# Performance work log

Measured on AMD Instinct MI355X. Metric: run time of the kernel, lower is better.

The kernel has to match this reference:

```python
import jax, jax.numpy as jnp
import numpy as np

N = 262144
D = 1024
H = 512
B = 512  # number of bags / segments


def setup_inputs() -> dict:
    key = jax.random.key(0)
    k1, k2, k3, k4, k5 = jax.random.split(key, 5)
    x = jax.random.normal(k1, (N, D), dtype=jnp.float32)
    batch = jnp.sort(jax.random.randint(k2, (N,), 0, B, dtype=jnp.int64))
    s1 = 1.0 / np.sqrt(D)
    s3 = 1.0 / np.sqrt(H)
    W1 = jax.random.uniform(k3, (H, D), dtype=jnp.float32, minval=-s1, maxval=s1)
    W2 = jax.random.uniform(k4, (H, D), dtype=jnp.float32, minval=-s1, maxval=s1)
    W3 = jax.random.uniform(k5, (1, H), dtype=jnp.float32, minval=-s3, maxval=s3)
    return {"x": x, "batch": batch, "W1": W1, "W2": W2, "W3": W3}


def reference(x, batch, W1, W2, W3):
    # gated attention logits: tanh(x W1^T) * softmax_over_h(x W2^T) -> W3
    ux = jnp.tanh(x @ W1.T)                       # (n, h)
    vx = jax.nn.softmax(x @ W2.T, axis=1)         # (n, h), Softmax(dim=1)
    alpha = (ux * vx) @ W3.T                      # (n, 1)

    # segment-wise stable softmax over instances within each bag
    a = alpha[:, 0]                               # (n,)
    seg_max = jax.ops.segment_max(a, batch, num_segments=B)   # (B,)
    e = jnp.exp(a - seg_max[batch])               # (n,)
    seg_sum = jax.ops.segment_sum(e, batch, num_segments=B)   # (B,)
    w = e / seg_sum[batch]                        # (n,)

    # weighted segment add-pool: (B, d)
    z = jax.ops.segment_sum(x * w[:, None], batch, num_segments=B)
    return z
```

## Files before the change

### kernel.cpp

```cpp
#include <hip/hip_runtime.h>
#include <stdint.h>

#define N_ROWS 262144
#define D_DIM  1024
#define H_DIM  512
#define N_SEG  512

typedef __attribute__((ext_vector_type(4)))  float  f32x4;
typedef __attribute__((ext_vector_type(8)))  __bf16 bf16x8;
typedef __attribute__((ext_vector_type(8)))  unsigned short u16x8;

static __device__ __forceinline__ unsigned short c2bf(float f) {
  union { __bf16 b; unsigned short u; } c; c.b = (__bf16)f; return c.u;
}
static __device__ __forceinline__ float fast_tanh(float u) {
  return 1.0f - 2.0f / (__expf(2.0f * u) + 1.0f);
}

__global__ void cvt_w(const float* __restrict__ W1, const float* __restrict__ W2,
                      unsigned short* __restrict__ wbf) {
  int gid = blockIdx.x * 256 + threadIdx.x;
  int l   = gid & 63;
  int cfi = (gid >> 6) & 15;
  int kt  = (gid >> 10) & 31;
  int hs  = gid >> 15;
  int c   = (cfi << 4) + (l & 15);
  int h   = (hs << 7) + (c >> 1);
  int k0  = (kt << 5) + ((l >> 4) << 3);
  const float* src = ((c & 1) ? W2 : W1) + h * 1024 + k0;
  f32x4 f0 = *(const f32x4*)src;
  f32x4 f1 = *(const f32x4*)(src + 4);
  u16x8 v;
  v[0]=c2bf(f0[0]); v[1]=c2bf(f0[1]); v[2]=c2bf(f0[2]); v[3]=c2bf(f0[3]);
  v[4]=c2bf(f1[0]); v[5]=c2bf(f1[1]); v[6]=c2bf(f1[2]); v[7]=c2bf(f1[3]);
  *(u16x8*)(wbf + (size_t)gid * 8) = v;
}

#define MF(A, B, C) __builtin_amdgcn_mfma_f32_16x16x32_bf16((A), (B), (C), 0, 0, 0)

#define STAGEB(KT, BOFF) do { \
  __builtin_amdgcn_global_load_lds( \
    (const __attribute__((address_space(1))) void*)(wsrc + ((uint32_t)(KT) << 13)), \
    (__attribute__((address_space(3))) void*)(lds + (BOFF) + (wid << 11)), 16, 0, 0); \
  __builtin_amdgcn_global_load_lds( \
    (const __attribute__((address_space(1))) void*)(wsrc + ((uint32_t)(KT) << 13) + 512), \
    (__attribute__((address_space(3))) void*)(lds + (BOFF) + (wid << 11) + 1024), 16, 0, 0); \
} while (0)

#define ALOAD(KT) do { \
  rA0 = *(const f32x4*)(xsrc + ((KT) << 5)); \
  rA1 = *(const f32x4*)(xsrc + ((KT) << 5) + 4); \
} while (0)

#define PACKA(BOFF) do { \
  u16x8 va; \
  va[0]=c2bf(rA0[0]); va[1]=c2bf(rA0[1]); va[2]=c2bf(rA0[2]); va[3]=c2bf(rA0[3]); \
  va[4]=c2bf(rA1[0]); va[5]=c2bf(rA1[1]); va[6]=c2bf(rA1[2]); va[7]=c2bf(rA1[3]); \
  *(u16x8*)(lds + (BOFF) + (tid << 4)) = va; \
} while (0)

#define COMPUTE(ABUF, BBUF) do { \
  bf16x8 bf_[4], af[4]; \
  _Pragma("unroll") \
  for (int fc = 0; fc < 4; ++fc) \
    bf_[fc] = *(const bf16x8*)(lds + (BBUF) + (((cg << 2) + fc) << 10) + (lane << 4)); \
  _Pragma("unroll") \
  for (int fr = 0; fr < 4; ++fr) \
    af[fr] = *(const bf16x8*)(lds + (ABUF) + (((rg << 2) + fr) << 10) + (lane << 4)); \
  __builtin_amdgcn_s_setprio(1); \
  _Pragma("unroll") \
  for (int fr = 0; fr < 4; ++fr) \
    _Pragma("unroll") \
    for (int fc = 0; fc < 4; ++fc) \
      acc[fr][fc] = MF(af[fr], bf_[fc], acc[fr][fc]); \
  __builtin_amdgcn_s_setprio(0); \
} while (0)

#define BAR2() do { \
  asm volatile("s_waitcnt vmcnt(2) lgkmcnt(0)" ::: "memory"); \
  __builtin_amdgcn_s_barrier(); \
} while (0)
#define BAR0() do { \
  asm volatile("s_waitcnt vmcnt(0) lgkmcnt(0)" ::: "memory"); \
  __builtin_amdgcn_s_barrier(); \
} while (0)

__launch_bounds__(512, 4)
__global__ void alpha_kernel(const float* __restrict__ x,
                             const unsigned short* __restrict__ wbf,
                             const float* __restrict__ W3,
                             float* __restrict__ pm, float* __restrict__ ps,
                             float* __restrict__ pn)
{
  __shared__ unsigned char lds[49152];
  const int tid  = threadIdx.x;
  const int lane = tid & 63;
  const int wid  = tid >> 6;
  const int rg   = wid >> 2;
  const int cg   = wid & 3;
  const int l15  = lane & 15;
  const int lg   = lane >> 4;
  const int bid  = blockIdx.x;
  const int rt   = ((bid >> 5) << 3) + (bid & 7);
  const int hs   = (bid >> 3) & 3;
  const int row0 = rt << 7;

  const float* xsrc = x + (size_t)(row0 + ((tid >> 6) << 4) + (tid & 15)) * 1024
                        + (((tid >> 4) & 3) << 3);

  const unsigned short* wsrc = wbf + ((uint32_t)hs << 18) + ((uint32_t)wid << 10) + ((uint32_t)lane << 3);

  f32x4 acc[4][4];
  #pragma unroll
  for (int fr = 0; fr < 4; ++fr)
    #pragma unroll
    for (int fc = 0; fc < 4; ++fc) acc[fr][fc] = (f32x4){0.f, 0.f, 0.f, 0.f};

  f32x4 rA0, rA1;

  STAGEB(0, 16384);
  ALOAD(0);
  PACKA(0);
  ALOAD(1);
  BAR2();

  #pragma unroll 1
  for (int kt = 0; kt < 30; kt += 2) {
    STAGEB(kt + 1, 32768);
    COMPUTE(0, 16384);
    PACKA(8192);
    ALOAD(kt + 2);
    BAR2();
    STAGEB(kt + 2, 16384);
    COMPUTE(8192, 32768);
    PACKA(0);
    ALOAD(kt + 3);
    BAR2();
  }
  STAGEB(31, 32768);
  COMPUTE(0, 16384);
  PACKA(8192);
  BAR0();
  COMPUTE(8192, 32768);

  float w3v[4];
  #pragma unroll
  for (int fc = 0; fc < 4; ++fc)
    w3v[fc] = W3[(hs << 7) + (((cg << 6) + (fc << 4) + l15) >> 1)];

  float* pmb = (float*)(lds);
  float* psb = pmb + 512;
  float* pnb = psb + 512;

  #pragma unroll
  for (int fr = 0; fr < 4; ++fr) {
    f32x4 mv, sv, nv;
    #pragma unroll
    for (int j = 0; j < 4; ++j) {
      float g0 = fast_tanh(acc[fr][0][j]) * w3v[0];
      float g1 = fast_tanh(acc[fr][1][j]) * w3v[1];
      float g2 = fast_tanh(acc[fr][2][j]) * w3v[2];
      float g3 = fast_tanh(acc[fr][3][j]) * w3v[3];
      float gs0 = __shfl_xor(g0, 1);
      float gs1 = __shfl_xor(g1, 1);
      float gs2 = __shfl_xor(g2, 1);
      float gs3 = __shfl_xor(g3, 1);
      float mj = fmaxf(fmaxf(acc[fr][0][j], acc[fr][1][j]),
                       fmaxf(acc[fr][2][j], acc[fr][3][j]));
      mj = fmaxf(mj, __shfl_xor(mj, 2));
      mj = fmaxf(mj, __shfl_xor(mj, 4));
      mj = fmaxf(mj, __shfl_xor(mj, 8));
      float p0 = __expf(acc[fr][0][j] - mj);
      float p1 = __expf(acc[fr][1][j] - mj);
      float p2 = __expf(acc[fr][2][j] - mj);
      float p3 = __expf(acc[fr][3][j] - mj);
      float sj = p0 + p1 + p2 + p3;
      float nj = gs0 * p0 + gs1 * p1 + gs2 * p2 + gs3 * p3;
      sj += __shfl_xor(sj, 2); nj += __shfl_xor(nj, 2);
      sj += __shfl_xor(sj, 4); nj += __shfl_xor(nj, 4);
      sj += __shfl_xor(sj, 8); nj += __shfl_xor(nj, 8);
      mv[j] = mj; sv[j] = sj; nv[j] = nj;
    }
    if (l15 == 1) {
      int idx = (cg << 7) + (rg << 6) + (fr << 4) + (lg << 2);
      *(f32x4*)&pmb[idx] = mv;
      *(f32x4*)&psb[idx] = sv;
      *(f32x4*)&pnb[idx] = nv;
    }
  }
  __syncthreads();
  if (tid < 128) {
    float m0 = pmb[tid], m1 = pmb[128 + tid], m2 = pmb[256 + tid], m3 = pmb[384 + tid];
    float M = fmaxf(fmaxf(m0, m1), fmaxf(m2, m3));
    float e0 = __expf(m0 - M), e1 = __expf(m1 - M), e2 = __expf(m2 - M), e3 = __expf(m3 - M);
    float S  = psb[tid]*e0 + psb[128+tid]*e1 + psb[256+tid]*e2 + psb[384+tid]*e3;
    float Nn = pnb[tid]*e0 + pnb[128+tid]*e1 + pnb[256+tid]*e2 + pnb[384+tid]*e3;
    size_t r = (size_t)(row0 + tid);
    pm[r * 4 + hs] = M;
    ps[r * 4 + hs] = S;
    pn[r * 4 + hs] = Nn;
  }
}

__global__ void combine_a(const float* __restrict__ pm, const float* __restrict__ ps,
                          const float* __restrict__ pn, float* __restrict__ a) {
  size_t r = (size_t)blockIdx.x * 256 + threadIdx.x;
  float M = -3.4e38f;
  #pragma unroll
  for (int s = 0; s < 4; ++s) M = fmaxf(M, pm[r * 4 + s]);
  float S = 0.f, Nn = 0.f;
  #pragma unroll
  for (int s = 0; s < 4; ++s) {
    float e = __expf(pm[r * 4 + s] - M);
    S  += ps[r * 4 + s] * e;
    Nn += pn[r * 4 + s] * e;
  }
  a[r] = Nn / S;
}

static __device__ __forceinline__ int lower_bound(const int* __restrict__ batch, int key) {
  int lo = 0, hi = N_ROWS;
  while (lo < hi) { int mid = (lo + hi) >> 1; if (batch[mid] < key) lo = mid + 1; else hi = mid; }
  return lo;
}

__global__ void seg_kernel(const float* __restrict__ a, const int* __restrict__ batch,
                           float* __restrict__ w) {
  __shared__ float sm[8];
  int b = blockIdx.x;
  int start = lower_bound(batch, b);
  int end   = lower_bound(batch, b + 1);
  int tid = threadIdx.x;

  float m = -3.4e38f;
  for (int i = start + tid; i < end; i += 256) m = fmaxf(m, a[i]);
  for (int d = 1; d < 64; d <<= 1) m = fmaxf(m, __shfl_xor(m, d));
  if ((tid & 63) == 0) sm[tid >> 6] = m;
  __syncthreads();
  m = fmaxf(fmaxf(sm[0], sm[1]), fmaxf(sm[2], sm[3]));

  float s = 0.f;
  for (int i = start + tid; i < end; i += 256) s += __expf(a[i] - m);
  for (int d = 1; d < 64; d <<= 1) s += __shfl_xor(s, d);
  if ((tid & 63) == 0) sm[4 + (tid >> 6)] = s;
  __syncthreads();
  s = sm[4] + sm[5] + sm[6] + sm[7];

  float rinv = 1.0f / s;
  for (int i = start + tid; i < end; i += 256) w[i] = __expf(a[i] - m) * rinv;
}

__global__ void z_kernel(const float* __restrict__ x, const float* __restrict__ w,
                         const int* __restrict__ batch, float* __restrict__ z) {
  int b = blockIdx.x >> 2, part = blockIdx.x & 3;
  int start = lower_bound(batch, b);
  int end   = lower_bound(batch, b + 1);
  int len = end - start;
  int ps = start + ((len * part) >> 2);
  int pe = start + ((len * (part + 1)) >> 2);
  int col = threadIdx.x << 2;

  f32x4 acc = (f32x4){0.f, 0.f, 0.f, 0.f};
  for (int i = ps; i < pe; ++i) {
    f32x4 xv = *(const f32x4*)(x + ((size_t)i << 10) + col);
    float wi = w[i];
    acc += xv * wi;
  }
  float* zp = z + ((size_t)b << 10) + col;
  atomicAdd(zp + 0, acc[0]);
  atomicAdd(zp + 1, acc[1]);
  atomicAdd(zp + 2, acc[2]);
  atomicAdd(zp + 3, acc[3]);
}

extern "C" void kernel_launch(void* const* d_in, const int* in_sizes, int n_in,
                              void* d_out, int out_size, void* d_ws, size_t ws_size,
                              hipStream_t stream) {
  const float* x     = (const float*)d_in[0];
  const int*   batch = (const int*)d_in[1];
  const float* W1    = (const float*)d_in[2];
  const float* W2    = (const float*)d_in[3];
  const float* W3    = (const float*)d_in[4];
  float* z = (float*)d_out;

  unsigned short* wbf = (unsigned short*)d_ws;
  float* a  = (float*)((char*)d_ws + (2u << 20));
  float* w  = (float*)((char*)d_ws + (3u << 20));
  float* pm = (float*)((char*)d_ws + (4u << 20));
  float* ps = (float*)((char*)d_ws + (8u << 20));
  float* pn = (float*)((char*)d_ws + (12u << 20));

  (void)hipMemsetAsync(d_out, 0, (size_t)N_SEG * D_DIM * sizeof(float), stream);

  cvt_w<<<512, 256, 0, stream>>>(W1, W2, wbf);

  alpha_kernel<<<8192, 512, 0, stream>>>(x, wbf, W3, pm, ps, pn);

  combine_a<<<N_ROWS / 256, 256, 0, stream>>>(pm, ps, pn, a);

  seg_kernel<<<N_SEG, 256, 0, stream>>>(a, batch, w);

  z_kernel<<<N_SEG * 4, 256, 0, stream>>>(x, w, batch, z);
}
```

Before: 1.035 ms.

## Split each K-step into two barrier-ping-ponged MFMA half-phases interleaved with loads

Restructures the main GEMM loop so each K-tile is processed in two halves: load B fragments and half of A, issue the next B stage, run 8 MFMAs, then load the rest of A, pack and issue the next A global load, and run the remaining 8 MFMAs. Extra s_barriers are inserted around each half to create a ping-pong schedule where waves alternate between memory and MFMA work. The goal is better overlap of LDS and global traffic with matrix compute, at the cost of more barriers and finer-grained synchronization that could stall waves.

```diff
diff --git a/kernel.cpp b/kernel.cpp
--- a/kernel.cpp
+++ b/kernel.cpp
@@ -59,14 +59,43 @@
   *(u16x8*)(lds + (BOFF) + (tid << 4)) = va; \
 } while (0)
 
+#define LDB(BUF, FC) (*(const bf16x8*)(lds + (BUF) + (((cg << 2) + (FC)) << 10) + (lane << 4)))
+#define LDA(BUF, FR) (*(const bf16x8*)(lds + (BUF) + (((rg << 2) + (FR)) << 10) + (lane << 4)))
+
+#define PHASE(ABUF, BBUF, AOTH, BOTH, KT) do { \
+  bf16x8 bf0 = LDB(BBUF, 0), bf1 = LDB(BBUF, 1), bf2 = LDB(BBUF, 2), bf3 = LDB(BBUF, 3); \
+  bf16x8 a0 = LDA(ABUF, 0), a1 = LDA(ABUF, 1); \
+  STAGEB((KT) + 1, BOTH); \
+  __builtin_amdgcn_s_barrier(); \
+  asm volatile("s_waitcnt lgkmcnt(0)" ::: "memory"); \
+  __builtin_amdgcn_s_setprio(1); \
+  acc[0][0] = MF(a0, bf0, acc[0][0]); acc[0][1] = MF(a0, bf1, acc[0][1]); \
+  acc[0][2] = MF(a0, bf2, acc[0][2]); acc[0][3] = MF(a0, bf3, acc[0][3]); \
+  acc[1][0] = MF(a1, bf0, acc[1][0]); acc[1][1] = MF(a1, bf1, acc[1][1]); \
+  acc[1][2] = MF(a1, bf2, acc[1][2]); acc[1][3] = MF(a1, bf3, acc[1][3]); \
+  __builtin_amdgcn_s_setprio(0); \
+  __builtin_amdgcn_s_barrier(); \
+  bf16x8 a2 = LDA(ABUF, 2), a3 = LDA(ABUF, 3); \
+  PACKA(AOTH); \
+  ALOAD((KT) + 2); \
+  __builtin_amdgcn_s_barrier(); \
+  asm volatile("s_waitcnt lgkmcnt(0)" ::: "memory"); \
+  __builtin_amdgcn_s_setprio(1); \
+  acc[2][0] = MF(a2, bf0, acc[2][0]); acc[2][1] = MF(a2, bf1, acc[2][1]); \
+  acc[2][2] = MF(a2, bf2, acc[2][2]); acc[2][3] = MF(a2, bf3, acc[2][3]); \
+  acc[3][0] = MF(a3, bf0, acc[3][0]); acc[3][1] = MF(a3, bf1, acc[3][1]); \
+  acc[3][2] = MF(a3, bf2, acc[3][2]); acc[3][3] = MF(a3, bf3, acc[3][3]); \
+  __builtin_amdgcn_s_setprio(0); \
+  asm volatile("s_waitcnt vmcnt(2)" ::: "memory"); \
+  __builtin_amdgcn_s_barrier(); \
+} while (0)
+
 #define COMPUTE(ABUF, BBUF) do { \
   bf16x8 bf_[4], af[4]; \
   _Pragma("unroll") \
-  for (int fc = 0; fc < 4; ++fc) \
-    bf_[fc] = *(const bf16x8*)(lds + (BBUF) + (((cg << 2) + fc) << 10) + (lane << 4)); \
+  for (int fc = 0; fc < 4; ++fc) bf_[fc] = LDB(BBUF, fc); \
   _Pragma("unroll") \
-  for (int fr = 0; fr < 4; ++fr) \
-    af[fr] = *(const bf16x8*)(lds + (ABUF) + (((rg << 2) + fr) << 10) + (lane << 4)); \
+  for (int fr = 0; fr < 4; ++fr) af[fr] = LDA(ABUF, fr); \
   __builtin_amdgcn_s_setprio(1); \
   _Pragma("unroll") \
   for (int fr = 0; fr < 4; ++fr) \
@@ -76,10 +105,6 @@
   __builtin_amdgcn_s_setprio(0); \
 } while (0)
 
-#define BAR2() do { \
-  asm volatile("s_waitcnt vmcnt(2) lgkmcnt(0)" ::: "memory"); \
-  __builtin_amdgcn_s_barrier(); \
-} while (0)
 #define BAR0() do { \
   asm volatile("s_waitcnt vmcnt(0) lgkmcnt(0)" ::: "memory"); \
   __builtin_amdgcn_s_barrier(); \
@@ -122,20 +147,13 @@
   ALOAD(0);
   PACKA(0);
   ALOAD(1);
-  BAR2();
+  asm volatile("s_waitcnt vmcnt(2) lgkmcnt(0)" ::: "memory");
+  __builtin_amdgcn_s_barrier();
 
   #pragma unroll 1
   for (int kt = 0; kt < 30; kt += 2) {
-    STAGEB(kt + 1, 32768);
-    COMPUTE(0, 16384);
-    PACKA(8192);
-    ALOAD(kt + 2);
-    BAR2();
-    STAGEB(kt + 2, 16384);
-    COMPUTE(8192, 32768);
-    PACKA(0);
-    ALOAD(kt + 3);
-    BAR2();
+    PHASE(0,    16384, 8192, 32768, kt);
+    PHASE(8192, 32768, 0,    16384, kt + 1);
   }
   STAGEB(31, 32768);
   COMPUTE(0, 16384);
```

After: 1.057 ms. +2.2%, slower.

## Pre-convert x to swizzled bf16 chunks and use 256-row tiles with triple-buffered DMA

Applied to the files above, without the earlier changes.

Adds a cvt_x pass that converts x in 16 chunks to bf16 in a swizzled tile layout, so the GEMM kernel can stage A via direct global-to-LDS loads instead of register load plus convert plus LDS store. The new alpha_fast kernel uses 256-row tiles (8x4 MFMA fragments per wave), 96KB dynamic LDS with triple buffering, and occupancy 2, which roughly halves redundant B traffic per row. The cost is an extra read of x in fp32 and a write and re-read of the bf16 copy, plus 32 extra launches. It only runs when the workspace is at least 56MB; otherwise the old kernel is used.

```diff
diff --git a/kernel.cpp b/kernel.cpp
--- a/kernel.cpp
+++ b/kernel.cpp
@@ -36,6 +36,27 @@
   *(u16x8*)(wbf + (size_t)gid * 8) = v;
 }
 
+__global__ void cvt_x(const float* __restrict__ x, unsigned short* __restrict__ ximg,
+                      int chunk) {
+  int gid = blockIdx.x * 256 + threadIdx.x;
+  int s   = gid & 1023;
+  int kt  = (gid >> 10) & 31;
+  int rtl = gid >> 15;
+  int f   = s >> 6;
+  int j   = s & 63;
+  int r4  = j >> 2;
+  int c   = j & 3;
+  int row = (((chunk << 6) + rtl) << 8) + (f << 4) + r4;
+  int k0  = (kt << 5) + ((c ^ (r4 & 3)) << 3);
+  const float* src = x + (size_t)row * 1024 + k0;
+  f32x4 f0 = *(const f32x4*)src;
+  f32x4 f1 = *(const f32x4*)(src + 4);
+  u16x8 v;
+  v[0]=c2bf(f0[0]); v[1]=c2bf(f0[1]); v[2]=c2bf(f0[2]); v[3]=c2bf(f0[3]);
+  v[4]=c2bf(f1[0]); v[5]=c2bf(f1[1]); v[6]=c2bf(f1[2]); v[7]=c2bf(f1[3]);
+  *(u16x8*)(ximg + (size_t)gid * 8) = v;
+}
+
 #define MF(A, B, C) __builtin_amdgcn_mfma_f32_16x16x32_bf16((A), (B), (C), 0, 0, 0)
 
 #define STAGEB(KT, BOFF) do { \
@@ -47,26 +68,175 @@
     (__attribute__((address_space(3))) void*)(lds + (BOFF) + (wid << 11) + 1024), 16, 0, 0); \
 } while (0)
 
-#define ALOAD(KT) do { \
+#define LDB(BUF, FC) (*(const bf16x8*)(lds + (BUF) + (((cg << 2) + (FC)) << 10) + (lane << 4)))
+
+#define FAST_A0 0
+#define FAST_A1 16384
+#define FAST_A2 32768
+#define FAST_B0 49152
+#define FAST_B1 65536
+#define FAST_B2 81920
+
+#define STAGEA(KT, AOFF) do { \
+  __builtin_amdgcn_global_load_lds( \
+    (const __attribute__((address_space(1))) void*)(asrc + ((uint32_t)(KT) << 13)), \
+    (__attribute__((address_space(3))) void*)(lds + (AOFF) + (wid << 10)), 16, 0, 0); \
+  __builtin_amdgcn_global_load_lds( \
+    (const __attribute__((address_space(1))) void*)(asrc + ((uint32_t)(KT) << 13) + 4096), \
+    (__attribute__((address_space(3))) void*)(lds + (AOFF) + (wid << 10) + 8192), 16, 0, 0); \
+} while (0)
+
+#define LDA8(BUF, FR) (*(const bf16x8*)(lds + (BUF) + (((rg << 3) + (FR)) << 10) + abase))
+
+#define MFQ16(FB, A0_, A1_, A2_, A3_) do { \
+  acc[(FB)+0][0]=MF(A0_,b0,acc[(FB)+0][0]); acc[(FB)+0][1]=MF(A0_,b1,acc[(FB)+0][1]); \
+  acc[(FB)+0][2]=MF(A0_,b2,acc[(FB)+0][2]); acc[(FB)+0][3]=MF(A0_,b3,acc[(FB)+0][3]); \
+  acc[(FB)+1][0]=MF(A1_,b0,acc[(FB)+1][0]); acc[(FB)+1][1]=MF(A1_,b1,acc[(FB)+1][1]); \
+  acc[(FB)+1][2]=MF(A1_,b2,acc[(FB)+1][2]); acc[(FB)+1][3]=MF(A1_,b3,acc[(FB)+1][3]); \
+  acc[(FB)+2][0]=MF(A2_,b0,acc[(FB)+2][0]); acc[(FB)+2][1]=MF(A2_,b1,acc[(FB)+2][1]); \
+  acc[(FB)+2][2]=MF(A2_,b2,acc[(FB)+2][2]); acc[(FB)+2][3]=MF(A2_,b3,acc[(FB)+2][3]); \
+  acc[(FB)+3][0]=MF(A3_,b0,acc[(FB)+3][0]); acc[(FB)+3][1]=MF(A3_,b1,acc[(FB)+3][1]); \
+  acc[(FB)+3][2]=MF(A3_,b2,acc[(FB)+3][2]); acc[(FB)+3][3]=MF(A3_,b3,acc[(FB)+3][3]); \
+} while (0)
+
+#define KTILE(RA, RB, SA, SB, KT, DOSTAGE, VMSTR) do { \
+  bf16x8 b0 = LDB(RB,0), b1 = LDB(RB,1), b2 = LDB(RB,2), b3 = LDB(RB,3); \
+  bf16x8 a0 = LDA8(RA,0), a1 = LDA8(RA,1), a2 = LDA8(RA,2), a3 = LDA8(RA,3); \
+  if (DOSTAGE) { STAGEA((KT)+2, SA); STAGEB((KT)+2, SB); } \
+  __builtin_amdgcn_s_barrier(); \
+  asm volatile("s_waitcnt lgkmcnt(0)" ::: "memory"); \
+  __builtin_amdgcn_s_setprio(1); MFQ16(0, a0, a1, a2, a3); __builtin_amdgcn_s_setprio(0); \
+  __builtin_amdgcn_s_barrier(); \
+  bf16x8 a4 = LDA8(RA,4), a5 = LDA8(RA,5), a6 = LDA8(RA,6), a7 = LDA8(RA,7); \
+  __builtin_amdgcn_s_barrier(); \
+  asm volatile("s_waitcnt lgkmcnt(0)" ::: "memory"); \
+  __builtin_amdgcn_s_setprio(1); MFQ16(4, a4, a5, a6, a7); __builtin_amdgcn_s_setprio(0); \
+  asm volatile("s_waitcnt vmcnt(" VMSTR ")" ::: "memory"); \
+  __builtin_amdgcn_s_barrier(); \
+} while (0)
+
+__launch_bounds__(512, 2)
+__global__ void alpha_fast(const unsigned short* __restrict__ ximg,
+                           const unsigned short* __restrict__ wbf,
+                           const float* __restrict__ W3,
+                           float* __restrict__ pm, float* __restrict__ ps,
+                           float* __restrict__ pn, int chunk)
+{
+  extern __shared__ unsigned char lds[];
+  const int tid  = threadIdx.x;
+  const int lane = tid & 63;
+  const int wid  = tid >> 6;
+  const int rg   = wid >> 2;
+  const int cg   = wid & 3;
+  const int l15  = lane & 15;
+  const int lg   = lane >> 4;
+  const int bid  = blockIdx.x;
+  const int rtl  = ((bid >> 5) << 3) + (bid & 7);
+  const int hs   = (bid >> 3) & 3;
+  const int rt   = (chunk << 6) + rtl;
+  const int row0 = rt << 8;
+
+  const unsigned short* asrc = ximg + ((size_t)rtl << 18) + ((uint32_t)tid << 3);
+  const unsigned short* wsrc = wbf + ((uint32_t)hs << 18) + ((uint32_t)wid << 10) + ((uint32_t)lane << 3);
+
+  const uint32_t abase = ((uint32_t)l15 << 6) + (((uint32_t)(lg ^ (l15 & 3))) << 4);
+
+  f32x4 acc[8][4];
+  #pragma unroll
+  for (int fr = 0; fr < 8; ++fr)
+    #pragma unroll
+    for (int fc = 0; fc < 4; ++fc) acc[fr][fc] = (f32x4){0.f, 0.f, 0.f, 0.f};
+
+  STAGEA(0, FAST_A0); STAGEB(0, FAST_B0);
+  STAGEA(1, FAST_A1); STAGEB(1, FAST_B1);
+  asm volatile("s_waitcnt vmcnt(4)" ::: "memory");
+  __builtin_amdgcn_s_barrier();
+
+  #pragma unroll 1
+  for (int kt = 0; kt < 30; kt += 3) {
+    KTILE(FAST_A0, FAST_B0, FAST_A2, FAST_B2, kt,     1, "4");
+    KTILE(FAST_A1, FAST_B1, FAST_A0, FAST_B0, kt + 1, 1, "4");
+    KTILE(FAST_A2, FAST_B2, FAST_A1, FAST_B1, kt + 2, 1, "4");
+  }
+  KTILE(FAST_A0, FAST_B0, FAST_A2, FAST_B2, 30, 0, "0");
+  KTILE(FAST_A1, FAST_B1, FAST_A2, FAST_B2, 31, 0, "0");
+
+  float w3v[4];
+  #pragma unroll
+  for (int fc = 0; fc < 4; ++fc)
+    w3v[fc] = W3[(hs << 7) + (((cg << 6) + (fc << 4) + l15) >> 1)];
+
+  float* pmb = (float*)(lds);
+  float* psb = pmb + 1024;
+  float* pnb = psb + 1024;
+
+  #pragma unroll
+  for (int fr = 0; fr < 8; ++fr) {
+    f32x4 mv, sv, nv;
+    #pragma unroll
+    for (int j = 0; j < 4; ++j) {
+      float g0 = fast_tanh(acc[fr][0][j]) * w3v[0];
+      float g1 = fast_tanh(acc[fr][1][j]) * w3v[1];
+      float g2 = fast_tanh(acc[fr][2][j]) * w3v[2];
+      float g3 = fast_tanh(acc[fr][3][j]) * w3v[3];
+      float gs0 = __shfl_xor(g0, 1);
+      float gs1 = __shfl_xor(g1, 1);
+      float gs2 = __shfl_xor(g2, 1);
+      float gs3 = __shfl_xor(g3, 1);
+      float mj = fmaxf(fmaxf(acc[fr][0][j], acc[fr][1][j]),
+                       fmaxf(acc[fr][2][j], acc[fr][3][j]));
+      mj = fmaxf(mj, __shfl_xor(mj, 2));
+      mj = fmaxf(mj, __shfl_xor(mj, 4));
+      mj = fmaxf(mj, __shfl_xor(mj, 8));
+      float p0 = __expf(acc[fr][0][j] - mj);
+      float p1 = __expf(acc[fr][1][j] - mj);
+      float p2 = __expf(acc[fr][2][j] - mj);
+      float p3 = __expf(acc[fr][3][j] - mj);
+      float sj = p0 + p1 + p2 + p3;
+      float nj = gs0 * p0 + gs1 * p1 + gs2 * p2 + gs3 * p3;
+      sj += __shfl_xor(sj, 2); nj += __shfl_xor(nj, 2);
+      sj += __shfl_xor(sj, 4); nj += __shfl_xor(nj, 4);
+      sj += __shfl_xor(sj, 8); nj += __shfl_xor(nj, 8);
+      mv[j] = mj; sv[j] = sj; nv[j] = nj;
+    }
+    if (l15 == 1) {
+      int idx = (cg << 8) + (rg << 7) + (fr << 4) + (lg << 2);
+      *(f32x4*)&pmb[idx] = mv;
+      *(f32x4*)&psb[idx] = sv;
+      *(f32x4*)&pnb[idx] = nv;
+    }
+  }
+  __syncthreads();
+  if (tid < 256) {
+    float m0 = pmb[tid], m1 = pmb[256 + tid], m2 = pmb[512 + tid], m3 = pmb[768 + tid];
+    float M = fmaxf(fmaxf(m0, m1), fmaxf(m2, m3));
+    float e0 = __expf(m0 - M), e1 = __expf(m1 - M), e2 = __expf(m2 - M), e3 = __expf(m3 - M);
+    float S  = psb[tid]*e0 + psb[256+tid]*e1 + psb[512+tid]*e2 + psb[768+tid]*e3;
+    float Nn = pnb[tid]*e0 + pnb[256+tid]*e1 + pnb[512+tid]*e2 + pnb[768+tid]*e3;
+    size_t r = (size_t)(row0 + tid);
+    pm[r * 4 + hs] = M;
+    ps[r * 4 + hs] = S;
+    pn[r * 4 + hs] = Nn;
+  }
+}
+
+#define FB_ALOAD(KT) do { \
   rA0 = *(const f32x4*)(xsrc + ((KT) << 5)); \
   rA1 = *(const f32x4*)(xsrc + ((KT) << 5) + 4); \
 } while (0)
-
-#define PACKA(BOFF) do { \
+#define FB_PACKA(BOFF) do { \
   u16x8 va; \
   va[0]=c2bf(rA0[0]); va[1]=c2bf(rA0[1]); va[2]=c2bf(rA0[2]); va[3]=c2bf(rA0[3]); \
   va[4]=c2bf(rA1[0]); va[5]=c2bf(rA1[1]); va[6]=c2bf(rA1[2]); va[7]=c2bf(rA1[3]); \
   *(u16x8*)(lds + (BOFF) + (tid << 4)) = va; \
 } while (0)
-
-#define COMPUTE(ABUF, BBUF) do { \
+#define FB_LDA(BUF, FR) (*(const bf16x8*)(lds + (BUF) + (((rg << 2) + (FR)) << 10) + (lane << 4)))
+#define FB_COMPUTE(ABUF, BBUF) do { \
   bf16x8 bf_[4], af[4]; \
   _Pragma("unroll") \
-  for (int fc = 0; fc < 4; ++fc) \
-    bf_[fc] = *(const bf16x8*)(lds + (BBUF) + (((cg << 2) + fc) << 10) + (lane << 4)); \
+  for (int fc = 0; fc < 4; ++fc) bf_[fc] = LDB(BBUF, fc); \
   _Pragma("unroll") \
-  for (int fr = 0; fr < 4; ++fr) \
-    af[fr] = *(const bf16x8*)(lds + (ABUF) + (((rg << 2) + fr) << 10) + (lane << 4)); \
+  for (int fr = 0; fr < 4; ++fr) af[fr] = FB_LDA(ABUF, fr); \
   __builtin_amdgcn_s_setprio(1); \
   _Pragma("unroll") \
   for (int fr = 0; fr < 4; ++fr) \
@@ -75,22 +245,21 @@
       acc[fr][fc] = MF(af[fr], bf_[fc], acc[fr][fc]); \
   __builtin_amdgcn_s_setprio(0); \
 } while (0)
-
-#define BAR2() do { \
+#define FB_BAR2() do { \
   asm volatile("s_waitcnt vmcnt(2) lgkmcnt(0)" ::: "memory"); \
   __builtin_amdgcn_s_barrier(); \
 } while (0)
-#define BAR0() do { \
+#define FB_BAR0() do { \
   asm volatile("s_waitcnt vmcnt(0) lgkmcnt(0)" ::: "memory"); \
   __builtin_amdgcn_s_barrier(); \
 } while (0)
 
 __launch_bounds__(512, 4)
-__global__ void alpha_kernel(const float* __restrict__ x,
-                             const unsigned short* __restrict__ wbf,
-                             const float* __restrict__ W3,
-                             float* __restrict__ pm, float* __restrict__ ps,
-                             float* __restrict__ pn)
+__global__ void alpha_fb(const float* __restrict__ x,
+                         const unsigned short* __restrict__ wbf,
+                         const float* __restrict__ W3,
+                         float* __restrict__ pm, float* __restrict__ ps,
+                         float* __restrict__ pn)
 {
   __shared__ unsigned char lds[49152];
   const int tid  = threadIdx.x;
@@ -107,7 +276,6 @@
 
   const float* xsrc = x + (size_t)(row0 + ((tid >> 6) << 4) + (tid & 15)) * 1024
                         + (((tid >> 4) & 3) << 3);
-
   const unsigned short* wsrc = wbf + ((uint32_t)hs << 18) + ((uint32_t)wid << 10) + ((uint32_t)lane << 3);
 
   f32x4 acc[4][4];
@@ -119,29 +287,29 @@
   f32x4 rA0, rA1;
 
   STAGEB(0, 16384);
-  ALOAD(0);
-  PACKA(0);
-  ALOAD(1);
-  BAR2();
+  FB_ALOAD(0);
+  FB_PACKA(0);
+  FB_ALOAD(1);
+  FB_BAR2();
 
   #pragma unroll 1
   for (int kt = 0; kt < 30; kt += 2) {
     STAGEB(kt + 1, 32768);
-    COMPUTE(0, 16384);
-    PACKA(8192);
-    ALOAD(kt + 2);
-    BAR2();
+    FB_COMPUTE(0, 16384);
+    FB_PACKA(8192);
+    FB_ALOAD(kt + 2);
+    FB_BAR2();
     STAGEB(kt + 2, 16384);
-    COMPUTE(8192, 32768);
-    PACKA(0);
-    ALOAD(kt + 3);
-    BAR2();
+    FB_COMPUTE(8192, 32768);
+    FB_PACKA(0);
+    FB_ALOAD(kt + 3);
+    FB_BAR2();
   }
   STAGEB(31, 32768);
-  COMPUTE(0, 16384);
-  PACKA(8192);
-  BAR0();
-  COMPUTE(8192, 32768);
+  FB_COMPUTE(0, 16384);
+  FB_PACKA(8192);
+  FB_BAR0();
+  FB_COMPUTE(8192, 32768);
 
   float w3v[4];
   #pragma unroll
@@ -283,18 +451,28 @@
   const float* W3    = (const float*)d_in[4];
   float* z = (float*)d_out;
 
-  unsigned short* wbf = (unsigned short*)d_ws;
+  unsigned short* wbf  = (unsigned short*)d_ws;
   float* a  = (float*)((char*)d_ws + (2u << 20));
   float* w  = (float*)((char*)d_ws + (3u << 20));
   float* pm = (float*)((char*)d_ws + (4u << 20));
   float* ps = (float*)((char*)d_ws + (8u << 20));
   float* pn = (float*)((char*)d_ws + (12u << 20));
+  unsigned short* ximg = (unsigned short*)((char*)d_ws + (16u << 20));
 
   (void)hipMemsetAsync(d_out, 0, (size_t)N_SEG * D_DIM * sizeof(float), stream);
 
   cvt_w<<<512, 256, 0, stream>>>(W1, W2, wbf);
 
-  alpha_kernel<<<8192, 512, 0, stream>>>(x, wbf, W3, pm, ps, pn);
+  if (ws_size >= ((size_t)56 << 20)) {
+    (void)hipFuncSetAttribute(reinterpret_cast<const void*>(alpha_fast),
+                              hipFuncAttributeMaxDynamicSharedMemorySize, 98304);
+    for (int c = 0; c < 16; ++c) {
+      cvt_x<<<8192, 256, 0, stream>>>(x, ximg, c);
+      alpha_fast<<<256, 512, 98304, stream>>>(ximg, wbf, W3, pm, ps, pn, c);
+    }
+  } else {
+    alpha_fb<<<8192, 512, 0, stream>>>(x, wbf, W3, pm, ps, pn);
+  }
 
   combine_a<<<N_ROWS / 256, 256, 0, stream>>>(pm, ps, pn, a);
 
```

Result: slower. 1.237 ms (+19.6%).

## Switch alpha GEMM to 32x32 MFMA with register-held weights and 8-way H split

Applied to the files above, without the earlier changes.

Rewrites the fused GEMM kernel to use 32x32x16 bf16 MFMA. Each wave loads its weight fragments straight from global memory into registers instead of staging them in LDS, and only the x tile is double-buffered in LDS with a single barrier per 64-wide K step. The H dimension is split into 8 slices instead of 4, which doubles the grid and the partial buffers, and occupancy is raised to 6 blocks per CU. The aim is fewer LDS round trips and barriers and better latency hiding. In exchange, each row tile of x is now read and converted twice as often, and the per-row combine does more work.

```diff
diff --git a/kernel.cpp b/kernel.cpp
--- a/kernel.cpp
+++ b/kernel.cpp
@@ -7,6 +7,7 @@
 #define N_SEG  512
 
 typedef __attribute__((ext_vector_type(4)))  float  f32x4;
+typedef __attribute__((ext_vector_type(16))) float  f32x16;
 typedef __attribute__((ext_vector_type(8)))  __bf16 bf16x8;
 typedef __attribute__((ext_vector_type(8)))  unsigned short u16x8;
 
@@ -21,12 +22,12 @@
                       unsigned short* __restrict__ wbf) {
   int gid = blockIdx.x * 256 + threadIdx.x;
   int l   = gid & 63;
-  int cfi = (gid >> 6) & 15;
-  int kt  = (gid >> 10) & 31;
-  int hs  = gid >> 15;
-  int c   = (cfi << 4) + (l & 15);
-  int h   = (hs << 7) + (c >> 1);
-  int k0  = (kt << 5) + ((l >> 4) << 3);
+  int cg  = (gid >> 6) & 3;
+  int kt  = (gid >> 8) & 63;
+  int hs  = gid >> 14;
+  int c   = (cg << 5) + (l & 31);
+  int h   = (hs << 6) + (c >> 1);
+  int k0  = (kt << 4) + ((l >> 5) << 3);
   const float* src = ((c & 1) ? W2 : W1) + h * 1024 + k0;
   f32x4 f0 = *(const f32x4*)src;
   f32x4 f1 = *(const f32x4*)(src + 4);
@@ -36,156 +37,134 @@
   *(u16x8*)(wbf + (size_t)gid * 8) = v;
 }
 
-#define MF(A, B, C) __builtin_amdgcn_mfma_f32_16x16x32_bf16((A), (B), (C), 0, 0, 0)
-
-#define STAGEB(KT, BOFF) do { \
-  __builtin_amdgcn_global_load_lds( \
-    (const __attribute__((address_space(1))) void*)(wsrc + ((uint32_t)(KT) << 13)), \
-    (__attribute__((address_space(3))) void*)(lds + (BOFF) + (wid << 11)), 16, 0, 0); \
-  __builtin_amdgcn_global_load_lds( \
-    (const __attribute__((address_space(1))) void*)(wsrc + ((uint32_t)(KT) << 13) + 512), \
-    (__attribute__((address_space(3))) void*)(lds + (BOFF) + (wid << 11) + 1024), 16, 0, 0); \
-} while (0)
-
-#define ALOAD(KT) do { \
-  rA0 = *(const f32x4*)(xsrc + ((KT) << 5)); \
-  rA1 = *(const f32x4*)(xsrc + ((KT) << 5) + 4); \
-} while (0)
-
-#define PACKA(BOFF) do { \
-  u16x8 va; \
-  va[0]=c2bf(rA0[0]); va[1]=c2bf(rA0[1]); va[2]=c2bf(rA0[2]); va[3]=c2bf(rA0[3]); \
-  va[4]=c2bf(rA1[0]); va[5]=c2bf(rA1[1]); va[6]=c2bf(rA1[2]); va[7]=c2bf(rA1[3]); \
-  *(u16x8*)(lds + (BOFF) + (tid << 4)) = va; \
-} while (0)
-
-#define COMPUTE(ABUF, BBUF) do { \
-  bf16x8 bf_[4], af[4]; \
-  _Pragma("unroll") \
-  for (int fc = 0; fc < 4; ++fc) \
-    bf_[fc] = *(const bf16x8*)(lds + (BBUF) + (((cg << 2) + fc) << 10) + (lane << 4)); \
-  _Pragma("unroll") \
-  for (int fr = 0; fr < 4; ++fr) \
-    af[fr] = *(const bf16x8*)(lds + (ABUF) + (((rg << 2) + fr) << 10) + (lane << 4)); \
+#define MF32(A, B, C) __builtin_amdgcn_mfma_f32_32x32x16_bf16((A), (B), (C), 0, 0, 0)
+
+#define ALOAD(T) do { \
+  const float* _p = xsrc + ((T) << 6); \
+  r0 = *(const f32x4*)_p; r1 = *(const f32x4*)(_p + 4); \
+  r2 = *(const f32x4*)(_p + 8); r3 = *(const f32x4*)(_p + 12); \
+} while (0)
+
+#define PACKA(BUF) do { \
+  u16x8 va, vb; \
+  va[0]=c2bf(r0[0]); va[1]=c2bf(r0[1]); va[2]=c2bf(r0[2]); va[3]=c2bf(r0[3]); \
+  va[4]=c2bf(r1[0]); va[5]=c2bf(r1[1]); va[6]=c2bf(r1[2]); va[7]=c2bf(r1[3]); \
+  vb[0]=c2bf(r2[0]); vb[1]=c2bf(r2[1]); vb[2]=c2bf(r2[2]); vb[3]=c2bf(r2[3]); \
+  vb[4]=c2bf(r3[0]); vb[5]=c2bf(r3[1]); vb[6]=c2bf(r3[2]); vb[7]=c2bf(r3[3]); \
+  *(u16x8*)(lds + (BUF) + wb0) = va; \
+  *(u16x8*)(lds + (BUF) + wb0 + 512) = vb; \
+} while (0)
+
+#define KST(KQ, BUF, WU, WL, KT) do { \
+  WL = *(const bf16x8*)(wsrc + ((uint32_t)((KT) + 1) << 11)); \
+  bf16x8 A0 = *(const bf16x8*)(lds + (BUF) + ((KQ) << 12) + ra); \
+  bf16x8 A1 = *(const bf16x8*)(lds + (BUF) + ((KQ) << 12) + ra + 1024); \
   __builtin_amdgcn_s_setprio(1); \
-  _Pragma("unroll") \
-  for (int fr = 0; fr < 4; ++fr) \
-    _Pragma("unroll") \
-    for (int fc = 0; fc < 4; ++fc) \
-      acc[fr][fc] = MF(af[fr], bf_[fc], acc[fr][fc]); \
+  acc0 = MF32(A0, WU, acc0); \
+  acc1 = MF32(A1, WU, acc1); \
   __builtin_amdgcn_s_setprio(0); \
 } while (0)
 
-#define BAR2() do { \
-  asm volatile("s_waitcnt vmcnt(2) lgkmcnt(0)" ::: "memory"); \
+#define ENDBAR() do { \
+  asm volatile("s_waitcnt lgkmcnt(0)" ::: "memory"); \
   __builtin_amdgcn_s_barrier(); \
 } while (0)
-#define BAR0() do { \
-  asm volatile("s_waitcnt vmcnt(0) lgkmcnt(0)" ::: "memory"); \
-  __builtin_amdgcn_s_barrier(); \
-} while (0)
-
-__launch_bounds__(512, 4)
+
+__launch_bounds__(512, 6)
 __global__ void alpha_kernel(const float* __restrict__ x,
                              const unsigned short* __restrict__ wbf,
                              const float* __restrict__ W3,
                              float* __restrict__ pm, float* __restrict__ ps,
                              float* __restrict__ pn)
 {
-  __shared__ unsigned char lds[49152];
+  __shared__ unsigned char lds[32768 + 6144];
   const int tid  = threadIdx.x;
   const int lane = tid & 63;
   const int wid  = tid >> 6;
   const int rg   = wid >> 2;
   const int cg   = wid & 3;
-  const int l15  = lane & 15;
-  const int lg   = lane >> 4;
+  const int l31  = lane & 31;
+  const int hi   = lane >> 5;
   const int bid  = blockIdx.x;
-  const int rt   = ((bid >> 5) << 3) + (bid & 7);
-  const int hs   = (bid >> 3) & 3;
+  const int rt   = ((bid >> 6) << 3) + (bid & 7);
+  const int hs   = (bid >> 3) & 7;
   const int row0 = rt << 7;
 
-  const float* xsrc = x + (size_t)(row0 + ((tid >> 6) << 4) + (tid & 15)) * 1024
-                        + (((tid >> 4) & 3) << 3);
-
-  const unsigned short* wsrc = wbf + ((uint32_t)hs << 18) + ((uint32_t)wid << 10) + ((uint32_t)lane << 3);
-
-  f32x4 acc[4][4];
-  #pragma unroll
-  for (int fr = 0; fr < 4; ++fr)
-    #pragma unroll
-    for (int fc = 0; fc < 4; ++fc) acc[fr][fc] = (f32x4){0.f, 0.f, 0.f, 0.f};
-
-  f32x4 rA0, rA1;
-
-  STAGEB(0, 16384);
+  const int ar = tid & 127;
+  const int akq = tid >> 7;
+  const float* xsrc = x + (size_t)(row0 + ar) * 1024 + (akq << 4);
+  const uint32_t wb0 = ((uint32_t)akq << 12) + ((uint32_t)(ar >> 5) << 10)
+                     + ((uint32_t)(ar & 31) << 4);
+
+  const unsigned short* wsrc =
+      wbf + ((((uint32_t)hs << 14) + ((uint32_t)cg << 6) + (uint32_t)lane) << 3);
+
+  const uint32_t ra = ((uint32_t)rg << 11) + ((uint32_t)lane << 4);
+
+  f32x16 acc0, acc1;
+  #pragma unroll
+  for (int i = 0; i < 16; ++i) { acc0[i] = 0.f; acc1[i] = 0.f; }
+
+  f32x4 r0, r1, r2, r3;
+  bf16x8 WA, WB;
+
   ALOAD(0);
   PACKA(0);
-  ALOAD(1);
-  BAR2();
+  WA = *(const bf16x8*)(wsrc);
+  ENDBAR();
 
   #pragma unroll 1
-  for (int kt = 0; kt < 30; kt += 2) {
-    STAGEB(kt + 1, 32768);
-    COMPUTE(0, 16384);
-    PACKA(8192);
-    ALOAD(kt + 2);
-    BAR2();
-    STAGEB(kt + 2, 16384);
-    COMPUTE(8192, 32768);
-    PACKA(0);
-    ALOAD(kt + 3);
-    BAR2();
-  }
-  STAGEB(31, 32768);
-  COMPUTE(0, 16384);
-  PACKA(8192);
-  BAR0();
-  COMPUTE(8192, 32768);
-
-  float w3v[4];
-  #pragma unroll
-  for (int fc = 0; fc < 4; ++fc)
-    w3v[fc] = W3[(hs << 7) + (((cg << 6) + (fc << 4) + l15) >> 1)];
-
-  float* pmb = (float*)(lds);
+  for (int t = 0; t < 16; ++t) {
+    const uint32_t bufc = (uint32_t)(t & 1) << 14;
+    const uint32_t bufn = bufc ^ 16384u;
+    if (t < 15) ALOAD(t + 1);
+    KST(0, bufc, WA, WB, t * 4 + 0);
+    KST(1, bufc, WB, WA, t * 4 + 1);
+    KST(2, bufc, WA, WB, t * 4 + 2);
+    KST(3, bufc, WB, WA, t * 4 + 3);
+    if (t < 15) PACKA(bufn);
+    ENDBAR();
+  }
+
+  float w3v = W3[(hs << 6) + (((cg << 5) + l31) >> 1)];
+  float* pmb = (float*)(lds + 32768);
   float* psb = pmb + 512;
   float* pnb = psb + 512;
 
   #pragma unroll
-  for (int fr = 0; fr < 4; ++fr) {
-    f32x4 mv, sv, nv;
-    #pragma unroll
-    for (int j = 0; j < 4; ++j) {
-      float g0 = fast_tanh(acc[fr][0][j]) * w3v[0];
-      float g1 = fast_tanh(acc[fr][1][j]) * w3v[1];
-      float g2 = fast_tanh(acc[fr][2][j]) * w3v[2];
-      float g3 = fast_tanh(acc[fr][3][j]) * w3v[3];
-      float gs0 = __shfl_xor(g0, 1);
-      float gs1 = __shfl_xor(g1, 1);
-      float gs2 = __shfl_xor(g2, 1);
-      float gs3 = __shfl_xor(g3, 1);
-      float mj = fmaxf(fmaxf(acc[fr][0][j], acc[fr][1][j]),
-                       fmaxf(acc[fr][2][j], acc[fr][3][j]));
-      mj = fmaxf(mj, __shfl_xor(mj, 2));
-      mj = fmaxf(mj, __shfl_xor(mj, 4));
-      mj = fmaxf(mj, __shfl_xor(mj, 8));
-      float p0 = __expf(acc[fr][0][j] - mj);
-      float p1 = __expf(acc[fr][1][j] - mj);
-      float p2 = __expf(acc[fr][2][j] - mj);
-      float p3 = __expf(acc[fr][3][j] - mj);
-      float sj = p0 + p1 + p2 + p3;
-      float nj = gs0 * p0 + gs1 * p1 + gs2 * p2 + gs3 * p3;
-      sj += __shfl_xor(sj, 2); nj += __shfl_xor(nj, 2);
-      sj += __shfl_xor(sj, 4); nj += __shfl_xor(nj, 4);
-      sj += __shfl_xor(sj, 8); nj += __shfl_xor(nj, 8);
-      mv[j] = mj; sv[j] = sj; nv[j] = nj;
+  for (int r = 0; r < 16; ++r) {
+    float g = fast_tanh(acc0[r]) * w3v;
+    float gs = __shfl_xor(g, 1);
+    float m = acc0[r];
+    m = fmaxf(m, __shfl_xor(m, 2)); m = fmaxf(m, __shfl_xor(m, 4));
+    m = fmaxf(m, __shfl_xor(m, 8)); m = fmaxf(m, __shfl_xor(m, 16));
+    float p = __expf(acc0[r] - m);
+    float s = p, n = gs * p;
+    s += __shfl_xor(s, 2); n += __shfl_xor(n, 2);
+    s += __shfl_xor(s, 4); n += __shfl_xor(n, 4);
+    s += __shfl_xor(s, 8); n += __shfl_xor(n, 8);
+    s += __shfl_xor(s, 16); n += __shfl_xor(n, 16);
+    if (l31 == 1) {
+      int row = (rg << 6) + (r & 3) + ((r >> 2) << 3) + (hi << 2);
+      pmb[(cg << 7) + row] = m; psb[(cg << 7) + row] = s; pnb[(cg << 7) + row] = n;
     }
-    if (l15 == 1) {
-      int idx = (cg << 7) + (rg << 6) + (fr << 4) + (lg << 2);
-      *(f32x4*)&pmb[idx] = mv;
-      *(f32x4*)&psb[idx] = sv;
-      *(f32x4*)&pnb[idx] = nv;
+  }
+  #pragma unroll
+  for (int r = 0; r < 16; ++r) {
+    float g = fast_tanh(acc1[r]) * w3v;
+    float gs = __shfl_xor(g, 1);
+    float m = acc1[r];
+    m = fmaxf(m, __shfl_xor(m, 2)); m = fmaxf(m, __shfl_xor(m, 4));
+    m = fmaxf(m, __shfl_xor(m, 8)); m = fmaxf(m, __shfl_xor(m, 16));
+    float p = __expf(acc1[r] - m);
+    float s = p, n = gs * p;
+    s += __shfl_xor(s, 2); n += __shfl_xor(n, 2);
+    s += __shfl_xor(s, 4); n += __shfl_xor(n, 4);
+    s += __shfl_xor(s, 8); n += __shfl_xor(n, 8);
+    s += __shfl_xor(s, 16); n += __shfl_xor(n, 16);
+    if (l31 == 1) {
+      int row = (rg << 6) + 32 + (r & 3) + ((r >> 2) << 3) + (hi << 2);
+      pmb[(cg << 7) + row] = m; psb[(cg << 7) + row] = s; pnb[(cg << 7) + row] = n;
     }
   }
   __syncthreads();
@@ -196,9 +175,9 @@
     float S  = psb[tid]*e0 + psb[128+tid]*e1 + psb[256+tid]*e2 + psb[384+tid]*e3;
     float Nn = pnb[tid]*e0 + pnb[128+tid]*e1 + pnb[256+tid]*e2 + pnb[384+tid]*e3;
     size_t r = (size_t)(row0 + tid);
-    pm[r * 4 + hs] = M;
-    ps[r * 4 + hs] = S;
-    pn[r * 4 + hs] = Nn;
+    pm[r * 8 + hs] = M;
+    ps[r * 8 + hs] = S;
+    pn[r * 8 + hs] = Nn;
   }
 }
 
@@ -207,13 +186,13 @@
   size_t r = (size_t)blockIdx.x * 256 + threadIdx.x;
   float M = -3.4e38f;
   #pragma unroll
-  for (int s = 0; s < 4; ++s) M = fmaxf(M, pm[r * 4 + s]);
+  for (int s = 0; s < 8; ++s) M = fmaxf(M, pm[r * 8 + s]);
   float S = 0.f, Nn = 0.f;
   #pragma unroll
-  for (int s = 0; s < 4; ++s) {
-    float e = __expf(pm[r * 4 + s] - M);
-    S  += ps[r * 4 + s] * e;
-    Nn += pn[r * 4 + s] * e;
+  for (int s = 0; s < 8; ++s) {
+    float e = __expf(pm[r * 8 + s] - M);
+    S  += ps[r * 8 + s] * e;
+    Nn += pn[r * 8 + s] * e;
   }
   a[r] = Nn / S;
 }
@@ -287,14 +266,14 @@
   float* a  = (float*)((char*)d_ws + (2u << 20));
   float* w  = (float*)((char*)d_ws + (3u << 20));
   float* pm = (float*)((char*)d_ws + (4u << 20));
-  float* ps = (float*)((char*)d_ws + (8u << 20));
-  float* pn = (float*)((char*)d_ws + (12u << 20));
+  float* ps = (float*)((char*)d_ws + (12u << 20));
+  float* pn = (float*)((char*)d_ws + (20u << 20));
 
   (void)hipMemsetAsync(d_out, 0, (size_t)N_SEG * D_DIM * sizeof(float), stream);
 
   cvt_w<<<512, 256, 0, stream>>>(W1, W2, wbf);
 
-  alpha_kernel<<<8192, 512, 0, stream>>>(x, wbf, W3, pm, ps, pn);
+  alpha_kernel<<<16384, 512, 0, stream>>>(x, wbf, W3, pm, ps, pn);
 
   combine_a<<<N_ROWS / 256, 256, 0, stream>>>(pm, ps, pn, a);
 
```

Result: slower. 1.628 ms (+57.3%).
